# Optimization experiments

Hardware: AMD Instinct MI355X
Metric: run time of the kernel (lower is better)

The kernel has to match this reference:

```python
import jax, jax.numpy as jnp
import numpy as np

THETA = 10000.0

def _rope_cos_sin(seq_len, head_dim, dtype=jnp.float32):
    # matches precompute_freqs_cis: freqs over even indices of head_dim
    inv = 1.0 / (THETA ** (jnp.arange(0, head_dim, 2, dtype=jnp.float32) / head_dim))  # [hd/2]
    ang = jnp.arange(seq_len, dtype=jnp.float32)[:, None] * inv[None, :]               # [S, hd/2]
    return jnp.cos(ang).astype(dtype), jnp.sin(ang).astype(dtype)

def _apply_rope(x, cos, sin):
    # x: [b, h, s, d]; pairs are interleaved (d r) with r=2 -> complex (even=real, odd=imag)
    xe = x[..., 0::2]
    xo = x[..., 1::2]
    re = xe * cos - xo * sin
    im = xe * sin + xo * cos
    # interleave back: [..., d/2, 2] -> [..., d]
    return jnp.stack([re, im], axis=-1).reshape(x.shape)

def setup_inputs() -> dict:
    key = jax.random.key(0)
    ks = jax.random.split(key, 8)
    B, S, D = 2, 2048, 1024
    s = 0.02
    return {
        "query": jax.random.normal(ks[0], (B, S, D), jnp.float32),
        "key": jax.random.normal(ks[1], (B, S, D), jnp.float32),
        "value": jax.random.normal(ks[2], (B, S, D), jnp.float32),
        "q_w": jax.random.normal(ks[3], (D, D), jnp.float32) * s,
        "q_b": jnp.zeros((D,), jnp.float32),
        "k_w": jax.random.normal(ks[4], (D, D), jnp.float32) * s,
        "k_b": jnp.zeros((D,), jnp.float32),
        "v_w": jax.random.normal(ks[5], (D, D), jnp.float32) * s,
        "v_b": jnp.zeros((D,), jnp.float32),
        "o_w": jax.random.normal(ks[6], (D, D), jnp.float32) * s,
        "o_b": jnp.zeros((D,), jnp.float32),
    }

def reference(query, key, value, q_w, q_b, k_w, k_b, v_w, v_b, o_w, o_b):
    H = 16
    B, S, D = query.shape
    hd = D // H
    scaling = hd ** -0.5

    def split_heads(x):  # [b, s, (h d)] -> [b, h, s, d]
        return x.reshape(B, -1, H, hd).transpose(0, 2, 1, 3)

    q = split_heads(query @ q_w.T + q_b)
    k = split_heads(key @ k_w.T + k_b)
    v = split_heads(value @ v_w.T + v_b)

    cos, sin = _rope_cos_sin(S, hd)
    q = _apply_rope(q, cos, sin)
    k = _apply_rope(k, cos, sin)

    scores = jnp.einsum('bhqd,bhkd->bhqk', q, k) * scaling  # [B,H,S,S]
    attn = jax.nn.softmax(scores, axis=-1)
    out = jnp.einsum('bhqk,bhkd->bhqd', attn, v)            # [B,H,S,hd]
    out = out.transpose(0, 2, 1, 3).reshape(B, S, D)
    return out @ o_w.T + o_b
```

## Files before the change

### kernel.cpp

```cpp
#include <hip/hip_runtime.h>
#include <math.h>

#define B_  2
#define S_  2048
#define D_  1024
#define H_  16
#define HD_ 64
#define M_  (B_*S_)

typedef __attribute__((ext_vector_type(8))) short bf16x8;
typedef __attribute__((ext_vector_type(4))) float f32x4;
typedef unsigned short ushort_t;

#define MFMA32 __builtin_amdgcn_mfma_f32_16x16x32_bf16

__device__ inline unsigned short f2bf(float x) {
    unsigned u = __float_as_uint(x);
    unsigned r = (u + 0x7fff + ((u >> 16) & 1)) >> 16;
    return (unsigned short)r;
}
__device__ inline void gload16(const ushort_t* g, ushort_t* l) {
    __builtin_amdgcn_global_load_lds(
        (const __attribute__((address_space(1))) unsigned*)g,
        (__attribute__((address_space(3))) unsigned*)l, 16, 0, 0);
}

__global__ __launch_bounds__(256) void prep(
    const float* __restrict__ qa, const float* __restrict__ ka,
    const float* __restrict__ va,
    const float* __restrict__ qw, const float* __restrict__ kw,
    const float* __restrict__ vw, const float* __restrict__ ow,
    ushort_t* __restrict__ qab, ushort_t* __restrict__ kab,
    ushort_t* __restrict__ vab,
    ushort_t* __restrict__ qwb, ushort_t* __restrict__ kwb,
    ushort_t* __restrict__ vwb, ushort_t* __restrict__ owb,
    float* __restrict__ cost, float* __restrict__ sint)
{
    const int z = blockIdx.y;
    const int i = blockIdx.x * 256 + threadIdx.x;
    if (z == 7) {
        if (blockIdx.x >= (S_ * 32) / 256) return;
        int s = i >> 5, w = i & 31;
        double inv = pow(10000.0, -((double)(2 * w) / (double)HD_));
        double ang = (double)s * inv;
        double r = ang * 0.15915494309189535;
        r -= floor(r);
        float th = (float)r * 6.283185307179586f;
        cost[i] = __cosf(th);
        sint[i] = __sinf(th);
        return;
    }
    const float* in;
    ushort_t* dst;
    int n4;
    switch (z) {
        case 0: in = qa; dst = qab; n4 = (M_ * D_) / 4; break;
        case 1: in = ka; dst = kab; n4 = (M_ * D_) / 4; break;
        case 2: in = va; dst = vab; n4 = (M_ * D_) / 4; break;
        case 3: in = qw; dst = qwb; n4 = (D_ * D_) / 4; break;
        case 4: in = kw; dst = kwb; n4 = (D_ * D_) / 4; break;
        case 5: in = vw; dst = vwb; n4 = (D_ * D_) / 4; break;
        default: in = ow; dst = owb; n4 = (D_ * D_) / 4; break;
    }
    if (i >= n4) return;
    float4 v = ((const float4*)in)[i];
    unsigned short h0 = f2bf(v.x), h1 = f2bf(v.y), h2 = f2bf(v.z), h3 = f2bf(v.w);
    ((uint2*)dst)[i] = make_uint2((unsigned)h0 | ((unsigned)h1 << 16),
                                  (unsigned)h2 | ((unsigned)h3 << 16));
}

__global__ __launch_bounds__(256, 3) void fused_qkv(
    const ushort_t* __restrict__ A0, const ushort_t* __restrict__ A1,
    const ushort_t* __restrict__ A2,
    const ushort_t* __restrict__ W0, const ushort_t* __restrict__ W1,
    const ushort_t* __restrict__ W2,
    const float* __restrict__ b0, const float* __restrict__ b1,
    const float* __restrict__ b2,
    ushort_t* __restrict__ O0, ushort_t* __restrict__ O1,
    ushort_t* __restrict__ O2,
    const float* __restrict__ cost, const float* __restrict__ sint)
{
    __shared__ ushort_t Ab[12288];
    __shared__ ushort_t Wb[12288];

    const int tid  = threadIdx.x;
    const int wq   = tid >> 6;
    const int lane = tid & 63;
    const int l16  = lane & 15;
    const int quad = lane >> 4;

    const unsigned flat = blockIdx.x + (blockIdx.y << 3) + (blockIdx.z << 8);
    const unsigned xcd  = flat & 7;
    const unsigned slot = flat >> 3;
    const int z   = (int)(slot >> 5);
    const unsigned rr = slot & 31;
    const int bm  = (int)(xcd * 4 + (rr >> 3)) * 128;
    const int bn  = (int)(rr & 7) * 128;

    const ushort_t* A = z == 0 ? A0 : z == 1 ? A1 : A2;
    const ushort_t* W = z == 0 ? W0 : z == 1 ? W1 : W2;
    const float* bias = z == 0 ? b0 : z == 1 ? b1 : b2;

    const int m16 = tid & 15;
    const int akq = (tid >> 4) & 3;
    const int tw  = tid >> 6;

    const ushort_t* gA0 = A + (size_t)(bm + tw * 16 + m16) * D_ + akq * 8;
    const ushort_t* gA1 = gA0 + (size_t)64 * D_;
    const ushort_t* gW0 = W + (size_t)(bn + tw * 16 + m16) * D_ + akq * 8;
    const ushort_t* gW1 = gW0 + (size_t)64 * D_;

    const int wm = wq >> 1, wn = wq & 1;

    f32x4 acc[4][4];
#pragma unroll
    for (int mt = 0; mt < 4; ++mt)
#pragma unroll
        for (int nt = 0; nt < 4; ++nt)
            acc[mt][nt] = (f32x4){0.f, 0.f, 0.f, 0.f};

    gload16(gA0,      &Ab[tw * 512]);
    gload16(gA1,      &Ab[(tw + 4) * 512]);
    gload16(gW0,      &Wb[tw * 512]);
    gload16(gW1,      &Wb[(tw + 4) * 512]);
    gload16(gA0 + 32, &Ab[4096 + tw * 512]);
    gload16(gA1 + 32, &Ab[4096 + (tw + 4) * 512]);
    gload16(gW0 + 32, &Wb[4096 + tw * 512]);
    gload16(gW1 + 32, &Wb[4096 + (tw + 4) * 512]);

    int bcur = 0;
    for (int k = 0; k < 32; ++k) {
        if (k < 31) {
            asm volatile("s_waitcnt vmcnt(4)" ::: "memory");
        } else {
            asm volatile("s_waitcnt vmcnt(0)" ::: "memory");
        }
        __builtin_amdgcn_sched_barrier(0);
        __builtin_amdgcn_s_barrier();
        __builtin_amdgcn_sched_barrier(0);

        if (k < 30) {
            int bnx = bcur + 2; if (bnx >= 3) bnx -= 3;
            int ko = (k + 2) * 32;
            gload16(gA0 + ko, &Ab[bnx * 4096 + tw * 512]);
            gload16(gA1 + ko, &Ab[bnx * 4096 + (tw + 4) * 512]);
            gload16(gW0 + ko, &Wb[bnx * 4096 + tw * 512]);
            gload16(gW1 + ko, &Wb[bnx * 4096 + (tw + 4) * 512]);
        }

        const ushort_t* Abc = &Ab[bcur * 4096];
        const ushort_t* Wbc = &Wb[bcur * 4096];

        bf16x8 af[4], wf[4];
#pragma unroll
        for (int mt = 0; mt < 4; ++mt)
            af[mt] = *(const bf16x8*)&Abc[(wm * 4 + mt) * 512 + lane * 8];
#pragma unroll
        for (int nt = 0; nt < 4; ++nt)
            wf[nt] = *(const bf16x8*)&Wbc[(wn * 4 + nt) * 512 + lane * 8];
#pragma unroll
        for (int mt = 0; mt < 4; ++mt)
#pragma unroll
            for (int nt = 0; nt < 4; ++nt)
                acc[mt][nt] = MFMA32(af[mt], wf[nt], acc[mt][nt], 0, 0, 0);

        bcur += 1; if (bcur >= 3) bcur -= 3;
    }

    if (z == 0) {
        const float scale = 0.18033688011112042f;
#pragma unroll
        for (int mt = 0; mt < 4; ++mt) {
            int m = bm + wm * 64 + mt * 16 + quad * 4;
#pragma unroll
            for (int nt = 0; nt < 4; ++nt) {
                int n = bn + wn * 64 + nt * 16 + l16;
                float bb = bias[n];
                int h = n >> 6, d = n & 63, p = d >> 1;
#pragma unroll
                for (int r = 0; r < 4; ++r) {
                    int mm = m + r;
                    int s = mm & (S_ - 1), b = mm >> 11;
                    float x = acc[mt][nt][r] + bb;
                    float cs = cost[s * 32 + p], sn = sint[s * 32 + p];
                    float part = __shfl_xor(x, 1);
                    float y = (d & 1) ? (part * sn + x * cs)
                                      : (x * cs - part * sn);
                    O0[((size_t)(b * H_ + h) * S_ + s) * HD_ + d] = f2bf(y * scale);
                }
            }
        }
    } else if (z == 1) {
#pragma unroll
        for (int mt = 0; mt < 4; ++mt) {
            int m = bm + wm * 64 + mt * 16 + quad * 4;
#pragma unroll
            for (int nt = 0; nt < 4; ++nt) {
                int n = bn + wn * 64 + nt * 16 + l16;
                float bb = bias[n];
                int h = n >> 6, d = n & 63, p = d >> 1;
                int sub = ((d >> 5) & 1);
                int dq  = (d >> 3) & 3;
                int dj  = d & 7;
#pragma unroll
                for (int r = 0; r < 4; ++r) {
                    int mm = m + r;
                    int s = mm & (S_ - 1), b = mm >> 11;
                    float x = acc[mt][nt][r] + bb;
                    float cs = cost[s * 32 + p], sn = sint[s * 32 + p];
                    float part = __shfl_xor(x, 1);
                    float y = (d & 1) ? (part * sn + x * cs)
                                      : (x * cs - part * sn);
                    int kt  = s >> 5;
                    int st  = ((s >> 4) & 1) * 2 + sub;
                    size_t idx = ((size_t)(b * H_ + h) * 64 + kt) * 2048
                               + st * 512 + dq * 128 + (s & 15) * 8 + dj;
                    O1[idx] = f2bf(y);
                }
            }
        }
    } else {
#pragma unroll
        for (int mt = 0; mt < 4; ++mt) {
            int m = bm + wm * 64 + mt * 16 + quad * 4;
            int b = m >> 11, s0 = m & (S_ - 1);
            int vt = s0 >> 5;
            int kk = s0 & 31;
            int qd = (kk & 15) >> 2;
            int w0 = ((kk >> 4) & 1) * 4;
#pragma unroll
            for (int nt = 0; nt < 4; ++nt) {
                int n = bn + wn * 64 + nt * 16 + l16;
                float bb = bias[n];
                int h = n >> 6, d = n & 63;
                int mtv = d >> 4, dd = d & 15;
                unsigned short hh[4];
#pragma unroll
                for (int r = 0; r < 4; ++r)
                    hh[r] = f2bf(acc[mt][nt][r] + bb);
                size_t idx = ((size_t)(b * H_ + h) * 64 + vt) * 2048
                           + mtv * 512 + qd * 128 + dd * 8 + w0;
                *(uint2*)(O2 + idx) = make_uint2(
                    (unsigned)hh[0] | ((unsigned)hh[1] << 16),
                    (unsigned)hh[2] | ((unsigned)hh[3] << 16));
            }
        }
    }
}

__global__ __launch_bounds__(256, 2) void proj_o(
    const ushort_t* __restrict__ A, const ushort_t* __restrict__ W,
    const float* __restrict__ bias, float* __restrict__ outf)
{
    __shared__ ushort_t Ab[6144];
    __shared__ ushort_t Wb[12288];

    const int tid  = threadIdx.x;
    const int wq   = tid >> 6;
    const int lane = tid & 63;
    const int l16  = lane & 15;
    const int quad = lane >> 4;

    const unsigned flat = blockIdx.x + (blockIdx.y << 3);
    const unsigned xcd  = flat & 7;
    const unsigned slot = flat >> 3;
    const int bm = (int)(xcd * 8 + (slot >> 3)) * 64;
    const int bn = (int)(slot & 7) * 128;

    const int m16 = tid & 15;
    const int akq = (tid >> 4) & 3;
    const int tw  = tid >> 6;

    const ushort_t* gA  = A + (size_t)(bm + tw * 16 + m16) * D_ + akq * 8;
    const ushort_t* gW0 = W + (size_t)(bn + tw * 16 + m16) * D_ + akq * 8;
    const ushort_t* gW1 = gW0 + (size_t)64 * D_;

    const int wm = wq >> 1, wn = wq & 1;

    f32x4 acc[2][4];
#pragma unroll
    for (int mt = 0; mt < 2; ++mt)
#pragma unroll
        for (int nt = 0; nt < 4; ++nt)
            acc[mt][nt] = (f32x4){0.f, 0.f, 0.f, 0.f};

    gload16(gA,       &Ab[tw * 512]);
    gload16(gW0,      &Wb[tw * 512]);
    gload16(gW1,      &Wb[(tw + 4) * 512]);
    gload16(gA + 32,  &Ab[2048 + tw * 512]);
    gload16(gW0 + 32, &Wb[4096 + tw * 512]);
    gload16(gW1 + 32, &Wb[4096 + (tw + 4) * 512]);

    int bcur = 0;
    for (int k = 0; k < 32; ++k) {
        if (k < 31) {
            asm volatile("s_waitcnt vmcnt(3)" ::: "memory");
        } else {
            asm volatile("s_waitcnt vmcnt(0)" ::: "memory");
        }
        __builtin_amdgcn_sched_barrier(0);
        __builtin_amdgcn_s_barrier();
        __builtin_amdgcn_sched_barrier(0);

        if (k < 30) {
            int bnx = bcur + 2; if (bnx >= 3) bnx -= 3;
            int ko = (k + 2) * 32;
            gload16(gA  + ko, &Ab[bnx * 2048 + tw * 512]);
            gload16(gW0 + ko, &Wb[bnx * 4096 + tw * 512]);
            gload16(gW1 + ko, &Wb[bnx * 4096 + (tw + 4) * 512]);
        }

        const ushort_t* Abc = &Ab[bcur * 2048];
        const ushort_t* Wbc = &Wb[bcur * 4096];

        bf16x8 af[2], wf[4];
#pragma unroll
        for (int mt = 0; mt < 2; ++mt)
            af[mt] = *(const bf16x8*)&Abc[(wm * 2 + mt) * 512 + lane * 8];
#pragma unroll
        for (int nt = 0; nt < 4; ++nt)
            wf[nt] = *(const bf16x8*)&Wbc[(wn * 4 + nt) * 512 + lane * 8];
#pragma unroll
        for (int mt = 0; mt < 2; ++mt)
#pragma unroll
            for (int nt = 0; nt < 4; ++nt)
                acc[mt][nt] = MFMA32(af[mt], wf[nt], acc[mt][nt], 0, 0, 0);

        bcur += 1; if (bcur >= 3) bcur -= 3;
    }

#pragma unroll
    for (int mt = 0; mt < 2; ++mt) {
        int m = bm + wm * 32 + mt * 16 + quad * 4;
#pragma unroll
        for (int nt = 0; nt < 4; ++nt) {
            int n = bn + wn * 64 + nt * 16 + l16;
            float bb = bias[n];
#pragma unroll
            for (int r = 0; r < 4; ++r)
                outf[(size_t)(m + r) * D_ + n] = acc[mt][nt][r] + bb;
        }
    }
}

__device__ __forceinline__ void attn_body(
    bf16x8 (&KR)[4], bf16x8 (&VR)[4], int i,
    const bf16x8 (&qa)[4][2], f32x4 (&oacc)[4][4], f32x4 (&osum)[4],
    const bf16x8& ones8, const ushort_t* kp, const ushort_t* vp)
{
    f32x4 s[4][2];
#pragma unroll
    for (int nh = 0; nh < 4; ++nh)
#pragma unroll
        for (int g = 0; g < 2; ++g)
            s[nh][g] = (f32x4){0.f, 0.f, 0.f, 0.f};
    __builtin_amdgcn_s_setprio(1);
#pragma unroll
    for (int c = 0; c < 2; ++c)
#pragma unroll
        for (int nh = 0; nh < 4; ++nh)
#pragma unroll
            for (int g = 0; g < 2; ++g)
                s[nh][g] = MFMA32(KR[g * 2 + c], qa[nh][c], s[nh][g], 0, 0, 0);
    __builtin_amdgcn_s_setprio(0);

    bf16x8 pb8[4];
#pragma unroll
    for (int nh = 0; nh < 4; ++nh) {
        float p00 = __builtin_exp2f(s[nh][0][0]);
        float p01 = __builtin_exp2f(s[nh][0][1]);
        float p02 = __builtin_exp2f(s[nh][0][2]);
        float p03 = __builtin_exp2f(s[nh][0][3]);
        float p10 = __builtin_exp2f(s[nh][1][0]);
        float p11 = __builtin_exp2f(s[nh][1][1]);
        float p12 = __builtin_exp2f(s[nh][1][2]);
        float p13 = __builtin_exp2f(s[nh][1][3]);
        union { bf16x8 v; unsigned u[4]; } t;
        t.u[0] = __builtin_amdgcn_perm(__float_as_uint(p01),
                                       __float_as_uint(p00), 0x07060302);
        t.u[1] = __builtin_amdgcn_perm(__float_as_uint(p03),
                                       __float_as_uint(p02), 0x07060302);
        t.u[2] = __builtin_amdgcn_perm(__float_as_uint(p11),
                                       __float_as_uint(p10), 0x07060302);
        t.u[3] = __builtin_amdgcn_perm(__float_as_uint(p13),
                                       __float_as_uint(p12), 0x07060302);
        pb8[nh] = t.v;
    }

    __builtin_amdgcn_s_setprio(1);
#pragma unroll
    for (int mt = 0; mt < 4; ++mt)
#pragma unroll
        for (int nh = 0; nh < 4; ++nh)
            oacc[nh][mt] = MFMA32(VR[mt], pb8[nh], oacc[nh][mt], 0, 0, 0);
#pragma unroll
    for (int nh = 0; nh < 4; ++nh)
        osum[nh] = MFMA32(ones8, pb8[nh], osum[nh], 0, 0, 0);
    __builtin_amdgcn_s_setprio(0);

    if (i + 2 < 32) {
#pragma unroll
        for (int j = 0; j < 4; ++j) {
            KR[j] = *(const bf16x8*)(kp + (size_t)(i + 2) * 4096 + j * 512);
            VR[j] = *(const bf16x8*)(vp + (size_t)(i + 2) * 4096 + j * 512);
        }
    }
}

__global__ __launch_bounds__(256, 2) void attn_mfma(
    const ushort_t* __restrict__ Q, const ushort_t* __restrict__ Kf,
    const ushort_t* __restrict__ Vf, ushort_t* __restrict__ AO)
{
    __shared__ float MRG[128 * 65];
    __shared__ float PSB[128];

    const int tid  = threadIdx.x;
    const int wq   = tid >> 6;
    const int lane = tid & 63;
    const int l16  = lane & 15;
    const int quad = lane >> 4;
    const int qg   = wq & 1;
    const int ks   = wq >> 1;

    const unsigned flat = blockIdx.x + (blockIdx.y << 4);
    const unsigned xcd  = flat & 7;
    const unsigned slot = flat >> 3;
    const int bh   = (int)(xcd * 4 + (slot >> 4));
    const int q0   = (int)(slot & 15) * 128 + qg * 64;

    bf16x8 qa[4][2];
#pragma unroll
    for (int nh = 0; nh < 4; ++nh)
#pragma unroll
        for (int c = 0; c < 2; ++c) {
            int row = q0 + nh * 16 + l16;
            qa[nh][c] = *(const bf16x8*)(Q + ((size_t)bh * S_ + row) * HD_
                                           + c * 32 + quad * 8);
        }
#pragma unroll
    for (int nh = 0; nh < 4; ++nh)
#pragma unroll
        for (int c = 0; c < 2; ++c)
            asm volatile("" : "+v"(qa[nh][c]));

    f32x4 oacc[4][4];
    f32x4 osum[4];
#pragma unroll
    for (int nh = 0; nh < 4; ++nh) {
        osum[nh] = (f32x4){0.f, 0.f, 0.f, 0.f};
#pragma unroll
        for (int mt = 0; mt < 4; ++mt)
            oacc[nh][mt] = (f32x4){0.f, 0.f, 0.f, 0.f};
    }

    const bf16x8 ones8 = {(short)0x3F80, (short)0x3F80, (short)0x3F80,
                          (short)0x3F80, (short)0x3F80, (short)0x3F80,
                          (short)0x3F80, (short)0x3F80};

    const ushort_t* kp = Kf + (size_t)bh * 131072 + ks * 2048 + lane * 8;
    const ushort_t* vp = Vf + (size_t)bh * 131072 + ks * 2048 + lane * 8;

    bf16x8 kA[4], vA[4], kB[4], vB[4];
#pragma unroll
    for (int j = 0; j < 4; ++j) {
        kA[j] = *(const bf16x8*)(kp + j * 512);
        vA[j] = *(const bf16x8*)(vp + j * 512);
        kB[j] = *(const bf16x8*)(kp + 4096 + j * 512);
        vB[j] = *(const bf16x8*)(vp + 4096 + j * 512);
    }

    for (int i = 0; i < 32; i += 2) {
        attn_body(kA, vA, i,     qa, oacc, osum, ones8, kp, vp);
        attn_body(kB, vB, i + 1, qa, oacc, osum, ones8, kp, vp);
    }

    if (ks == 1) {
#pragma unroll
        for (int nh = 0; nh < 4; ++nh) {
#pragma unroll
            for (int mt = 0; mt < 4; ++mt)
#pragma unroll
                for (int r = 0; r < 4; ++r)
                    MRG[(qg * 64 + nh * 16 + l16) * 65 + mt * 16 + quad * 4 + r]
                        = oacc[nh][mt][r];
            if (quad == 0)
                PSB[qg * 64 + nh * 16 + l16] = osum[nh][0];
        }
    }
    __syncthreads();
    if (ks == 0) {
        const int b = bh >> 4, h = bh & 15;
#pragma unroll
        for (int nh = 0; nh < 4; ++nh) {
            float pst = osum[nh][0] + PSB[qg * 64 + nh * 16 + l16];
            float inv = 1.0f / pst;
            int q = q0 + nh * 16 + l16;
#pragma unroll
            for (int mt = 0; mt < 4; ++mt) {
                unsigned short hh[4];
#pragma unroll
                for (int r = 0; r < 4; ++r) {
                    float x = oacc[nh][mt][r]
                        + MRG[(qg * 64 + nh * 16 + l16) * 65 + mt * 16 + quad * 4 + r];
                    hh[r] = f2bf(x * inv);
                }
                size_t base = ((size_t)b * S_ + q) * D_ + h * HD_
                            + mt * 16 + quad * 4;
                *(uint2*)(AO + base) = make_uint2(
                    (unsigned)hh[0] | ((unsigned)hh[1] << 16),
                    (unsigned)hh[2] | ((unsigned)hh[3] << 16));
            }
        }
    }
}

extern "C" void kernel_launch(void* const* d_in, const int* in_sizes, int n_in,
                              void* d_out, int out_size, void* d_ws, size_t ws_size,
                              hipStream_t stream) {
    const float* query = (const float*)d_in[0];
    const float* key   = (const float*)d_in[1];
    const float* value = (const float*)d_in[2];
    const float* q_w   = (const float*)d_in[3];
    const float* q_b   = (const float*)d_in[4];
    const float* k_w   = (const float*)d_in[5];
    const float* k_b   = (const float*)d_in[6];
    const float* v_w   = (const float*)d_in[7];
    const float* v_b   = (const float*)d_in[8];
    const float* o_w   = (const float*)d_in[9];
    const float* o_b   = (const float*)d_in[10];
    float* out = (float*)d_out;

    const size_t NT = (size_t)M_ * D_;
    const size_t WT = (size_t)D_ * D_;
    ushort_t* p = (ushort_t*)d_ws;
    ushort_t* qa_b = p; p += NT;
    ushort_t* ka_b = p; p += NT;
    ushort_t* va_b = p; p += NT;
    ushort_t* wqb  = p; p += WT;
    ushort_t* wkb  = p; p += WT;
    ushort_t* wvb  = p; p += WT;
    ushort_t* wob  = p; p += WT;
    ushort_t* Qb   = p; p += NT;
    ushort_t* Kfr  = p; p += NT;
    ushort_t* Vfr  = p; p += NT;
    ushort_t* AO   = p; p += NT;
    float* cost = (float*)p;
    float* sint = cost + (size_t)S_ * 32;

    dim3 gp((unsigned)(NT / 4 / 256), 8);
    prep<<<gp, 256, 0, stream>>>(query, key, value, q_w, k_w, v_w, o_w,
                                 qa_b, ka_b, va_b, wqb, wkb, wvb, wob,
                                 cost, sint);

    dim3 gq(D_ / 128, M_ / 128, 3);
    fused_qkv<<<gq, 256, 0, stream>>>(
        qa_b, ka_b, va_b, wqb, wkb, wvb,
        q_b, k_b, v_b, Qb, Kfr, Vfr, cost, sint);

    dim3 agrid(S_ / 128, B_ * H_);
    attn_mfma<<<agrid, 256, 0, stream>>>(Qb, Kfr, Vfr, AO);

    dim3 go(D_ / 128, M_ / 64);
    proj_o<<<go, 256, 0, stream>>>(AO, wob, o_b, out);
}
```

Baseline: 245.4 us.

## Fuse fp32-to-bf16 activation conversion into QKV GEMM loads

```diff
diff --git a/kernel.cpp b/kernel.cpp
--- a/kernel.cpp
+++ b/kernel.cpp
@@ -26,19 +26,15 @@
 }
 
 __global__ __launch_bounds__(256) void prep(
-    const float* __restrict__ qa, const float* __restrict__ ka,
-    const float* __restrict__ va,
     const float* __restrict__ qw, const float* __restrict__ kw,
     const float* __restrict__ vw, const float* __restrict__ ow,
-    ushort_t* __restrict__ qab, ushort_t* __restrict__ kab,
-    ushort_t* __restrict__ vab,
     ushort_t* __restrict__ qwb, ushort_t* __restrict__ kwb,
     ushort_t* __restrict__ vwb, ushort_t* __restrict__ owb,
     float* __restrict__ cost, float* __restrict__ sint)
 {
     const int z = blockIdx.y;
     const int i = blockIdx.x * 256 + threadIdx.x;
-    if (z == 7) {
+    if (z == 4) {
         if (blockIdx.x >= (S_ * 32) / 256) return;
         int s = i >> 5, w = i & 31;
         double inv = pow(10000.0, -((double)(2 * w) / (double)HD_));
@@ -52,17 +48,13 @@
     }
     const float* in;
     ushort_t* dst;
-    int n4;
     switch (z) {
-        case 0: in = qa; dst = qab; n4 = (M_ * D_) / 4; break;
-        case 1: in = ka; dst = kab; n4 = (M_ * D_) / 4; break;
-        case 2: in = va; dst = vab; n4 = (M_ * D_) / 4; break;
-        case 3: in = qw; dst = qwb; n4 = (D_ * D_) / 4; break;
-        case 4: in = kw; dst = kwb; n4 = (D_ * D_) / 4; break;
-        case 5: in = vw; dst = vwb; n4 = (D_ * D_) / 4; break;
-        default: in = ow; dst = owb; n4 = (D_ * D_) / 4; break;
-    }
-    if (i >= n4) return;
+        case 0:  in = qw; dst = qwb; break;
+        case 1:  in = kw; dst = kwb; break;
+        case 2:  in = vw; dst = vwb; break;
+        default: in = ow; dst = owb; break;
+    }
+    if (i >= (D_ * D_) / 4) return;
     float4 v = ((const float4*)in)[i];
     unsigned short h0 = f2bf(v.x), h1 = f2bf(v.y), h2 = f2bf(v.z), h3 = f2bf(v.w);
     ((uint2*)dst)[i] = make_uint2((unsigned)h0 | ((unsigned)h1 << 16),
@@ -70,8 +62,8 @@
 }
 
 __global__ __launch_bounds__(256, 3) void fused_qkv(
-    const ushort_t* __restrict__ A0, const ushort_t* __restrict__ A1,
-    const ushort_t* __restrict__ A2,
+    const float* __restrict__ A0f, const float* __restrict__ A1f,
+    const float* __restrict__ A2f,
     const ushort_t* __restrict__ W0, const ushort_t* __restrict__ W1,
     const ushort_t* __restrict__ W2,
     const float* __restrict__ b0, const float* __restrict__ b1,
@@ -97,7 +89,7 @@
     const int bm  = (int)(xcd * 4 + (rr >> 3)) * 128;
     const int bn  = (int)(rr & 7) * 128;
 
-    const ushort_t* A = z == 0 ? A0 : z == 1 ? A1 : A2;
+    const float* Af = z == 0 ? A0f : z == 1 ? A1f : A2f;
     const ushort_t* W = z == 0 ? W0 : z == 1 ? W1 : W2;
     const float* bias = z == 0 ? b0 : z == 1 ? b1 : b2;
 
@@ -105,8 +97,8 @@
     const int akq = (tid >> 4) & 3;
     const int tw  = tid >> 6;
 
-    const ushort_t* gA0 = A + (size_t)(bm + tw * 16 + m16) * D_ + akq * 8;
-    const ushort_t* gA1 = gA0 + (size_t)64 * D_;
+    const float* gAf0 = Af + (size_t)(bm + tw * 16 + m16) * D_ + akq * 8;
+    const float* gAf1 = gAf0 + (size_t)64 * D_;
     const ushort_t* gW0 = W + (size_t)(bn + tw * 16 + m16) * D_ + akq * 8;
     const ushort_t* gW1 = gW0 + (size_t)64 * D_;
 
@@ -119,34 +111,53 @@
         for (int nt = 0; nt < 4; ++nt)
             acc[mt][nt] = (f32x4){0.f, 0.f, 0.f, 0.f};
 
-    gload16(gA0,      &Ab[tw * 512]);
-    gload16(gA1,      &Ab[(tw + 4) * 512]);
-    gload16(gW0,      &Wb[tw * 512]);
-    gload16(gW1,      &Wb[(tw + 4) * 512]);
-    gload16(gA0 + 32, &Ab[4096 + tw * 512]);
-    gload16(gA1 + 32, &Ab[4096 + (tw + 4) * 512]);
+    float4 cA0 = *(const float4*)(gAf0);
+    float4 cA1 = *(const float4*)(gAf0 + 4);
+    float4 cA2 = *(const float4*)(gAf1);
+    float4 cA3 = *(const float4*)(gAf1 + 4);
+    gload16(gW0, &Wb[tw * 512]);
+    gload16(gW1, &Wb[(tw + 4) * 512]);
+    float4 pA0 = *(const float4*)(gAf0 + 32);
+    float4 pA1 = *(const float4*)(gAf0 + 36);
+    float4 pA2 = *(const float4*)(gAf1 + 32);
+    float4 pA3 = *(const float4*)(gAf1 + 36);
     gload16(gW0 + 32, &Wb[4096 + tw * 512]);
     gload16(gW1 + 32, &Wb[4096 + (tw + 4) * 512]);
 
+    asm volatile("s_waitcnt vmcnt(6)" ::: "memory");
+    {
+        union { bf16x8 v; unsigned short s[8]; } t0, t1;
+        t0.s[0] = f2bf(cA0.x); t0.s[1] = f2bf(cA0.y);
+        t0.s[2] = f2bf(cA0.z); t0.s[3] = f2bf(cA0.w);
+        t0.s[4] = f2bf(cA1.x); t0.s[5] = f2bf(cA1.y);
+        t0.s[6] = f2bf(cA1.z); t0.s[7] = f2bf(cA1.w);
+        t1.s[0] = f2bf(cA2.x); t1.s[1] = f2bf(cA2.y);
+        t1.s[2] = f2bf(cA2.z); t1.s[3] = f2bf(cA2.w);
+        t1.s[4] = f2bf(cA3.x); t1.s[5] = f2bf(cA3.y);
+        t1.s[6] = f2bf(cA3.z); t1.s[7] = f2bf(cA3.w);
+        *(bf16x8*)&Ab[tw * 512 + lane * 8] = t0.v;
+        *(bf16x8*)&Ab[(tw + 4) * 512 + lane * 8] = t1.v;
+    }
+    asm volatile("s_waitcnt lgkmcnt(0)" ::: "memory");
+    __builtin_amdgcn_sched_barrier(0);
+
+    float4 nA0, nA1, nA2, nA3;
     int bcur = 0;
     for (int k = 0; k < 32; ++k) {
-        if (k < 31) {
-            asm volatile("s_waitcnt vmcnt(4)" ::: "memory");
-        } else {
-            asm volatile("s_waitcnt vmcnt(0)" ::: "memory");
-        }
-        __builtin_amdgcn_sched_barrier(0);
         __builtin_amdgcn_s_barrier();
         __builtin_amdgcn_sched_barrier(0);
 
         if (k < 30) {
+            int ko = (k + 2) * 32;
+            nA0 = *(const float4*)(gAf0 + ko);
+            nA1 = *(const float4*)(gAf0 + ko + 4);
+            nA2 = *(const float4*)(gAf1 + ko);
+            nA3 = *(const float4*)(gAf1 + ko + 4);
             int bnx = bcur + 2; if (bnx >= 3) bnx -= 3;
-            int ko = (k + 2) * 32;
-            gload16(gA0 + ko, &Ab[bnx * 4096 + tw * 512]);
-            gload16(gA1 + ko, &Ab[bnx * 4096 + (tw + 4) * 512]);
             gload16(gW0 + ko, &Wb[bnx * 4096 + tw * 512]);
             gload16(gW1 + ko, &Wb[bnx * 4096 + (tw + 4) * 512]);
         }
+        __builtin_amdgcn_sched_barrier(0);
 
         const ushort_t* Abc = &Ab[bcur * 4096];
         const ushort_t* Wbc = &Wb[bcur * 4096];
@@ -163,6 +174,30 @@
 #pragma unroll
             for (int nt = 0; nt < 4; ++nt)
                 acc[mt][nt] = MFMA32(af[mt], wf[nt], acc[mt][nt], 0, 0, 0);
+
+        __builtin_amdgcn_sched_barrier(0);
+        if (k < 31) {
+            if (k < 30) {
+                asm volatile("s_waitcnt vmcnt(6)" ::: "memory");
+            } else {
+                asm volatile("s_waitcnt vmcnt(0)" ::: "memory");
+            }
+            int bnw = bcur + 1; if (bnw >= 3) bnw -= 3;
+            union { bf16x8 v; unsigned short s[8]; } t0, t1;
+            t0.s[0] = f2bf(pA0.x); t0.s[1] = f2bf(pA0.y);
+            t0.s[2] = f2bf(pA0.z); t0.s[3] = f2bf(pA0.w);
+            t0.s[4] = f2bf(pA1.x); t0.s[5] = f2bf(pA1.y);
+            t0.s[6] = f2bf(pA1.z); t0.s[7] = f2bf(pA1.w);
+            t1.s[0] = f2bf(pA2.x); t1.s[1] = f2bf(pA2.y);
+            t1.s[2] = f2bf(pA2.z); t1.s[3] = f2bf(pA2.w);
+            t1.s[4] = f2bf(pA3.x); t1.s[5] = f2bf(pA3.y);
+            t1.s[6] = f2bf(pA3.z); t1.s[7] = f2bf(pA3.w);
+            *(bf16x8*)&Ab[bnw * 4096 + tw * 512 + lane * 8] = t0.v;
+            *(bf16x8*)&Ab[bnw * 4096 + (tw + 4) * 512 + lane * 8] = t1.v;
+            asm volatile("s_waitcnt lgkmcnt(0)" ::: "memory");
+            __builtin_amdgcn_sched_barrier(0);
+            pA0 = nA0; pA1 = nA1; pA2 = nA2; pA3 = nA3;
+        }
 
         bcur += 1; if (bcur >= 3) bcur -= 3;
     }
@@ -533,9 +568,6 @@
     const size_t NT = (size_t)M_ * D_;
     const size_t WT = (size_t)D_ * D_;
     ushort_t* p = (ushort_t*)d_ws;
-    ushort_t* qa_b = p; p += NT;
-    ushort_t* ka_b = p; p += NT;
-    ushort_t* va_b = p; p += NT;
     ushort_t* wqb  = p; p += WT;
     ushort_t* wkb  = p; p += WT;
     ushort_t* wvb  = p; p += WT;
@@ -547,14 +579,13 @@
     float* cost = (float*)p;
     float* sint = cost + (size_t)S_ * 32;
 
-    dim3 gp((unsigned)(NT / 4 / 256), 8);
-    prep<<<gp, 256, 0, stream>>>(query, key, value, q_w, k_w, v_w, o_w,
-                                 qa_b, ka_b, va_b, wqb, wkb, wvb, wob,
-                                 cost, sint);
+    dim3 gp((unsigned)((WT / 4) / 256), 5);
+    prep<<<gp, 256, 0, stream>>>(q_w, k_w, v_w, o_w,
+                                 wqb, wkb, wvb, wob, cost, sint);
 
     dim3 gq(D_ / 128, M_ / 128, 3);
     fused_qkv<<<gq, 256, 0, stream>>>(
-        qa_b, ka_b, va_b, wqb, wkb, wvb,
+        query, key, value, wqb, wkb, wvb,
         q_b, k_b, v_b, Qb, Kfr, Vfr, cost, sint);
 
     dim3 agrid(S_ / 128, B_ * H_);
```

Measured after the change: 262.3 us. 6.9% more time.
